# Performance work log

Measured on AMD Instinct MI355X. Metric: run time of the kernel, lower is better.

The kernel has to match this reference:

```python
import jax, jax.numpy as jnp
import numpy as np

KERNEL_EPSILON = 0.001


def setup_inputs() -> dict:
    key = jax.random.key(0)
    k1, k2, k3 = jax.random.split(key, 3)
    B, H, S, D = 4, 16, 4096, 64
    return {
        "query": jax.random.normal(k1, (B, H, S, D), dtype=jnp.float32),
        "key": jax.random.normal(k2, (B, H, S, D), dtype=jnp.float32),
        "value": jax.random.normal(k3, (B, H, S, D), dtype=jnp.float32),
        "mask": jnp.ones((B, S), dtype=jnp.float32),
    }


def reference(query, key, value, mask):
    # ReLU feature map + epsilon
    q = jax.nn.relu(query) + KERNEL_EPSILON          # [B,H,S,D]
    k = jax.nn.relu(key) + KERNEL_EPSILON            # [B,H,S,D]
    k = k * mask[:, None, :, None]                   # mask keys
    # kv: [B,H,D,E] = sum_s k[...,s,d] * v[...,s,e]  (done first: linear attention)
    kv = jnp.einsum("bhsd,bhse->bhde", k, value)
    numerator = jnp.einsum("bhsd,bhde->bhse", q, kv)  # [B,H,S,D]
    k_sum = jnp.sum(k, axis=-2)                       # [B,H,D]
    denominator = jnp.einsum("bhsd,bhd->bhs", q, k_sum)[..., None]
    return numerator / denominator
```

## Files before the change

kernel.cpp:

```cpp
#include <hip/hip_runtime.h>


namespace {
constexpr int kB = 4, kH = 16, kS = 4096, kD = 64;
constexpr int kBH = kB * kH;
constexpr float kEps = 0.001f;

constexpr int KVSZ = kD * kD;
constexpr int SEG  = KVSZ + kD;
constexpr int F4PS = SEG / 4;
}

__device__ __forceinline__ void async_cp16(const float* g, float* l) {
  __builtin_amdgcn_global_load_lds(
      (const __attribute__((address_space(1))) void*)g,
      (__attribute__((address_space(3))) void*)l, 16, 0, 0);
}

__global__ __launch_bounds__(256, 2)
void pa_kv_partial(const float* __restrict__ key, const float* __restrict__ value,
                   const float* __restrict__ mask, float* __restrict__ P, int ch1) {
  __shared__ float smemV[3 * 2048];
  __shared__ float smemK[4 * 512];
  __shared__ float msk[512];
  __shared__ float ksm[256];

  const int tid  = threadIdx.x;
  const int wid  = tid >> 6;
  const int lane = tid & 63;

  const int bh    = blockIdx.x / ch1;
  const int chunk = blockIdx.x - bh * ch1;
  const int b     = bh >> 4;
  const int rows  = kS / ch1;
  const int s0    = chunk * rows;
  const int tiles = rows >> 5;

  const float* kg = key   + (size_t)bh * kS * kD;
  const float* vg = value + (size_t)bh * kS * kD;
  const float* mb = mask  + (size_t)b * kS;

  for (int i = tid; i < rows; i += 256) msk[i] = mb[s0 + i];
  __syncthreads();

  float* ksT = smemK + wid * 512;
  float* v0b = smemV + wid * 512;
  float* v1b = smemV + 2048 + wid * 512;
  float* v2b = smemV + 4096 + wid * 512;

  const int lrow = lane >> 4;
  const int lcol = (lane & 15) << 2;
  const int ti   = lane >> 3;
  const int tj   = lane & 7;

  float acc[8][8];
#pragma unroll
  for (int i = 0; i < 8; ++i)
#pragma unroll
    for (int j = 0; j < 8; ++j) acc[i][j] = 0.f;
  float4 ksacc = make_float4(0.f, 0.f, 0.f, 0.f);

  const int r0 = wid * 8;
  float4 kqA0, kqA1, kqB0, kqB1;
  float mA0, mA1, mB0, mB1;

  async_cp16(vg + (size_t)(s0 + r0 + lrow) * kD + lcol, v0b);
  async_cp16(vg + (size_t)(s0 + r0 + 4 + lrow) * kD + lcol, v0b + 256);
  kqA0 = *(const float4*)(kg + (size_t)(s0 + r0 + lrow) * kD + lcol);
  kqA1 = *(const float4*)(kg + (size_t)(s0 + r0 + 4 + lrow) * kD + lcol);
  asm volatile("" ::: "memory");
  async_cp16(vg + (size_t)(s0 + r0 + 32 + lrow) * kD + lcol, v1b);
  async_cp16(vg + (size_t)(s0 + r0 + 36 + lrow) * kD + lcol, v1b + 256);
  kqB0 = *(const float4*)(kg + (size_t)(s0 + r0 + 32 + lrow) * kD + lcol);
  kqB1 = *(const float4*)(kg + (size_t)(s0 + r0 + 36 + lrow) * kD + lcol);
  asm volatile("" ::: "memory");
  mA0 = msk[r0 + lrow];      mA1 = msk[r0 + 4 + lrow];
  mB0 = msk[r0 + 32 + lrow]; mB1 = msk[r0 + 36 + lrow];

  int ts2 = s0 + r0 + 64;
  int to2 = r0 + 64;

#define PA_RND(KQ0, KQ1, M0, M1, WAITN, ISSUE)                                \
  {                                                                           \
    float4 kt0, kt1;                                                          \
    kt0.x = (fmaxf(KQ0.x, 0.f) + kEps) * M0;                                  \
    kt0.y = (fmaxf(KQ0.y, 0.f) + kEps) * M0;                                  \
    kt0.z = (fmaxf(KQ0.z, 0.f) + kEps) * M0;                                  \
    kt0.w = (fmaxf(KQ0.w, 0.f) + kEps) * M0;                                  \
    kt1.x = (fmaxf(KQ1.x, 0.f) + kEps) * M1;                                  \
    kt1.y = (fmaxf(KQ1.y, 0.f) + kEps) * M1;                                  \
    kt1.z = (fmaxf(KQ1.z, 0.f) + kEps) * M1;                                  \
    kt1.w = (fmaxf(KQ1.w, 0.f) + kEps) * M1;                                  \
    ksacc.x += kt0.x + kt1.x; ksacc.y += kt0.y + kt1.y;                       \
    ksacc.z += kt0.z + kt1.z; ksacc.w += kt0.w + kt1.w;                       \
    *(float4*)&ksT[lrow * 64 + lcol]       = kt0;                             \
    *(float4*)&ksT[(lrow + 4) * 64 + lcol] = kt1;                             \
    if (ISSUE) {                                                              \
      async_cp16(vg + (size_t)(ts2 + lrow) * kD + lcol, v2b);                 \
      async_cp16(vg + (size_t)(ts2 + 4 + lrow) * kD + lcol, v2b + 256);       \
      KQ0 = *(const float4*)(kg + (size_t)(ts2 + lrow) * kD + lcol);          \
      KQ1 = *(const float4*)(kg + (size_t)(ts2 + 4 + lrow) * kD + lcol);      \
      M0 = msk[to2 + lrow];  M1 = msk[to2 + 4 + lrow];                        \
      ts2 += 32; to2 += 32;                                                   \
    }                                                                         \
    asm volatile("s_waitcnt vmcnt(" #WAITN ")" ::: "memory");                 \
    _Pragma("unroll")                                                         \
    for (int ss = 0; ss < 8; ++ss) {                                          \
      const float4 kf0 = *(const float4*)&ksT[ss * 64 + 8 * ti];              \
      const float4 kf1 = *(const float4*)&ksT[ss * 64 + 8 * ti + 4];          \
      const float4 vf0 = *(const float4*)&v0b[ss * 64 + 8 * tj];              \
      const float4 vf1 = *(const float4*)&v0b[ss * 64 + 8 * tj + 4];          \
      const float ka[8] = {kf0.x, kf0.y, kf0.z, kf0.w,                        \
                           kf1.x, kf1.y, kf1.z, kf1.w};                       \
      const float va_[8] = {vf0.x, vf0.y, vf0.z, vf0.w,                       \
                            vf1.x, vf1.y, vf1.z, vf1.w};                      \
      _Pragma("unroll")                                                       \
      for (int i = 0; i < 8; ++i)                                             \
        _Pragma("unroll")                                                     \
        for (int j = 0; j < 8; ++j)                                           \
          acc[i][j] = fmaf(ka[i], va_[j], acc[i][j]);                         \
    }                                                                         \
    { float* rot_ = v0b; v0b = v1b; v1b = v2b; v2b = rot_; }                  \
  }

  for (int t = 0; t < tiles - 2; t += 2) {
    PA_RND(kqA0, kqA1, mA0, mA1, 8, true)
    PA_RND(kqB0, kqB1, mB0, mB1, 8, true)
  }
  PA_RND(kqA0, kqA1, mA0, mA1, 4, false)
  PA_RND(kqB0, kqB1, mB0, mB1, 0, false)
#undef PA_RND

  ksacc.x += __shfl_xor(ksacc.x, 16); ksacc.x += __shfl_xor(ksacc.x, 32);
  ksacc.y += __shfl_xor(ksacc.y, 16); ksacc.y += __shfl_xor(ksacc.y, 32);
  ksacc.z += __shfl_xor(ksacc.z, 16); ksacc.z += __shfl_xor(ksacc.z, 32);
  ksacc.w += __shfl_xor(ksacc.w, 16); ksacc.w += __shfl_xor(ksacc.w, 32);
  if (lane < 16) *(float4*)&ksm[wid * 64 + 4 * lane] = ksacc;

#pragma unroll
  for (int w = 0; w < 4; ++w) {
    __syncthreads();
    if (wid == w) {
#pragma unroll
      for (int i = 0; i < 8; ++i)
#pragma unroll
        for (int jj = 0; jj < 2; ++jj) {
          const int j = i * 2 + jj;
          float4 o = make_float4(acc[i][jj * 4 + 0], acc[i][jj * 4 + 1],
                                 acc[i][jj * 4 + 2], acc[i][jj * 4 + 3]);
          float* p = &smemV[(size_t)(j * 64 + lane) * 4];
          if (w != 0) {
            const float4 prev = *(const float4*)p;
            o.x += prev.x; o.y += prev.y; o.z += prev.z; o.w += prev.w;
          }
          *(float4*)p = o;
        }
    }
  }
  __syncthreads();

  float* Pd = P + (size_t)blockIdx.x * SEG;
#pragma unroll
  for (int i = 0; i < 4; ++i) {
    const int idx = tid + 256 * i;
    *(float4*)&Pd[(size_t)idx * 4] = *(const float4*)&smemV[(size_t)idx * 4];
  }
  if (tid < kD)
    Pd[KVSZ + tid] = ksm[tid] + ksm[64 + tid] + ksm[128 + tid] + ksm[192 + tid];
}

__global__ __launch_bounds__(256)
void pa_reduce(const float* __restrict__ P, float* __restrict__ R, int nseg) {
  const int gid = blockIdx.x * 256 + threadIdx.x;
  if (gid >= kBH * F4PS) return;
  const int bh  = gid / F4PS;
  const int pos = gid - bh * F4PS;

  const float* base = P + (size_t)bh * nseg * SEG + (size_t)pos * 4;
  float ax = 0.f, ay = 0.f, az = 0.f, aw = 0.f;
  for (int c = 0; c < nseg; ++c) {
    const float4 t = *(const float4*)(base + (size_t)c * SEG);
    ax += t.x; ay += t.y; az += t.z; aw += t.w;
  }

  int dpos;
  if (pos < KVSZ / 4) {
    const int j  = pos >> 6, ln = pos & 63;
    const int d  = 8 * (ln >> 3) + (j >> 1);
    const int e4 = 2 * (ln & 7) + (j & 1);
    dpos = d * 16 + e4;
  } else {
    dpos = pos;
  }
  *(float4*)&R[(size_t)bh * SEG + (size_t)dpos * 4] = make_float4(ax, ay, az, aw);
}

__global__ __launch_bounds__(256)
void pa_out(const float* __restrict__ query, const float* __restrict__ R,
            float* __restrict__ out) {
  __shared__ float ost[64 * 68];

  const int tid    = threadIdx.x;
  const int bh     = blockIdx.x >> 4;
  const int rowblk = blockIdx.x & 15;
  const int s      = rowblk * 256 + tid;

  const float* qrow = query + ((size_t)bh * kS + s) * kD;
  const float* Rb   = R + (size_t)bh * SEG;

  float4 acc[16];
#pragma unroll
  for (int e = 0; e < 16; ++e) acc[e] = make_float4(0.f, 0.f, 0.f, 0.f);
  float den = 0.f;

#pragma unroll 4
  for (int d4 = 0; d4 < 16; ++d4) {
    const float4 qv = *(const float4*)(qrow + 4 * d4);
    const float qd[4] = {fmaxf(qv.x, 0.f) + kEps, fmaxf(qv.y, 0.f) + kEps,
                         fmaxf(qv.z, 0.f) + kEps, fmaxf(qv.w, 0.f) + kEps};
#pragma unroll
    for (int dd = 0; dd < 4; ++dd) {
      const int d = 4 * d4 + dd;
      den = fmaf(qd[dd], Rb[KVSZ + d], den);
      const float* kvr = Rb + d * 64;
#pragma unroll
      for (int e = 0; e < 16; ++e) {
        acc[e].x = fmaf(qd[dd], kvr[4 * e + 0], acc[e].x);
        acc[e].y = fmaf(qd[dd], kvr[4 * e + 1], acc[e].y);
        acc[e].z = fmaf(qd[dd], kvr[4 * e + 2], acc[e].z);
        acc[e].w = fmaf(qd[dd], kvr[4 * e + 3], acc[e].w);
      }
    }
  }

  const float inv = 1.0f / den;
#pragma unroll
  for (int e = 0; e < 16; ++e) {
    acc[e].x *= inv; acc[e].y *= inv; acc[e].z *= inv; acc[e].w *= inv;
  }

  float* ob = out + ((size_t)bh * kS + (size_t)rowblk * 256) * kD;
  const int wid = tid >> 6, l = tid & 63;
  for (int bb = 0; bb < 4; ++bb) {
    if (wid == bb) {
#pragma unroll
      for (int e = 0; e < 16; ++e) *(float4*)&ost[l * 68 + 4 * e] = acc[e];
    }
    __syncthreads();
#pragma unroll
    for (int jj = 0; jj < 4; ++jj) {
      const int g = tid + 256 * jj;
      const int r = g >> 4, c = g & 15;
      *(float4*)&ob[(size_t)(bb * 64 + r) * kD + 4 * c] =
          *(const float4*)&ost[r * 68 + 4 * c];
    }
    __syncthreads();
  }
}

extern "C" void kernel_launch(void* const* d_in, const int* in_sizes, int n_in,
                              void* d_out, int out_size, void* d_ws, size_t ws_size,
                              hipStream_t stream) {
  const float* query = (const float*)d_in[0];
  const float* key   = (const float*)d_in[1];
  const float* value = (const float*)d_in[2];
  const float* mask  = (const float*)d_in[3];
  float* outp = (float*)d_out;

  auto need = [](int ch1) -> size_t {
    return (size_t)(kBH * ch1 + kBH) * SEG * sizeof(float);
  };
  int CH1 = 8;
  if (ws_size >= need(16)) CH1 = 16;

  float* P = (float*)d_ws;
  float* R = P + (size_t)kBH * CH1 * SEG;

  hipLaunchKernelGGL(pa_kv_partial, dim3(kBH * CH1), dim3(256), 0, stream,
                     key, value, mask, P, CH1);
  hipLaunchKernelGGL(pa_reduce, dim3((kBH * F4PS + 255) / 256), dim3(256), 0, stream,
                     P, R, CH1);
  hipLaunchKernelGGL(pa_out, dim3(kBH * 16), dim3(256), 0, stream,
                     query, R, outp);
}
```

Before: 282.0 us.

## Stream raw K and V via async LDS copies in a 4-deep per-wave ring

Replaces the register-staged key load plus LDS store with direct global-to-LDS async copies of both K and V into a 4-slot per-wave ring buffer of 16-row tiles. The ReLU, epsilon and mask transform moves into the inner FMA loop, where it is applied on the fly to values read from LDS. The key-sum becomes a per-lane scalar accumulation, so the shuffle reduction goes away. This removes VGPR staging and LDS write traffic and deepens prefetch, at the cost of redundant feature-map ALU work per outer-product step and an extra lgkmcnt wait before each issue.

```diff
diff --git a/kernel.cpp b/kernel.cpp
--- a/kernel.cpp
+++ b/kernel.cpp
@@ -20,8 +20,7 @@
 __global__ __launch_bounds__(256, 2)
 void pa_kv_partial(const float* __restrict__ key, const float* __restrict__ value,
                    const float* __restrict__ mask, float* __restrict__ P, int ch1) {
-  __shared__ float smemV[3 * 2048];
-  __shared__ float smemK[4 * 512];
+  __shared__ float smemU[8192];
   __shared__ float msk[512];
   __shared__ float ksm[256];
 
@@ -34,7 +33,7 @@
   const int b     = bh >> 4;
   const int rows  = kS / ch1;
   const int s0    = chunk * rows;
-  const int tiles = rows >> 5;
+  const int rounds = rows >> 4;
 
   const float* kg = key   + (size_t)bh * kS * kD;
   const float* vg = value + (size_t)bh * kS * kD;
@@ -43,75 +42,64 @@
   for (int i = tid; i < rows; i += 256) msk[i] = mb[s0 + i];
   __syncthreads();
 
-  float* ksT = smemK + wid * 512;
-  float* v0b = smemV + wid * 512;
-  float* v1b = smemV + 2048 + wid * 512;
-  float* v2b = smemV + 4096 + wid * 512;
-
-  const int lrow = lane >> 4;
-  const int lcol = (lane & 15) << 2;
-  const int ti   = lane >> 3;
-  const int tj   = lane & 7;
+  float* const ring = smemU + wid * 2048;
+#define RK(Pp) (ring + (Pp) * 512)
+#define RV(Pp) (ring + (Pp) * 512 + 256)
+
+  const int ti = lane >> 3;
+  const int tj = lane & 7;
+  const int rw = wid * 4;
 
   float acc[8][8];
 #pragma unroll
   for (int i = 0; i < 8; ++i)
 #pragma unroll
     for (int j = 0; j < 8; ++j) acc[i][j] = 0.f;
-  float4 ksacc = make_float4(0.f, 0.f, 0.f, 0.f);
-
-  const int r0 = wid * 8;
-  float4 kqA0, kqA1, kqB0, kqB1;
-  float mA0, mA1, mB0, mB1;
-
-  async_cp16(vg + (size_t)(s0 + r0 + lrow) * kD + lcol, v0b);
-  async_cp16(vg + (size_t)(s0 + r0 + 4 + lrow) * kD + lcol, v0b + 256);
-  kqA0 = *(const float4*)(kg + (size_t)(s0 + r0 + lrow) * kD + lcol);
-  kqA1 = *(const float4*)(kg + (size_t)(s0 + r0 + 4 + lrow) * kD + lcol);
-  asm volatile("" ::: "memory");
-  async_cp16(vg + (size_t)(s0 + r0 + 32 + lrow) * kD + lcol, v1b);
-  async_cp16(vg + (size_t)(s0 + r0 + 36 + lrow) * kD + lcol, v1b + 256);
-  kqB0 = *(const float4*)(kg + (size_t)(s0 + r0 + 32 + lrow) * kD + lcol);
-  kqB1 = *(const float4*)(kg + (size_t)(s0 + r0 + 36 + lrow) * kD + lcol);
-  asm volatile("" ::: "memory");
-  mA0 = msk[r0 + lrow];      mA1 = msk[r0 + 4 + lrow];
-  mB0 = msk[r0 + 32 + lrow]; mB1 = msk[r0 + 36 + lrow];
-
-  int ts2 = s0 + r0 + 64;
-  int to2 = r0 + 64;
-
-#define PA_RND(KQ0, KQ1, M0, M1, WAITN, ISSUE)                                \
+  float ksacc = 0.f;
+
+  {
+    const size_t g0 = (size_t)(s0 + rw) * kD + lane * 4;
+    async_cp16(kg + g0, RK(0));
+    async_cp16(vg + g0, RV(0));
+    asm volatile("" ::: "memory");
+    async_cp16(kg + g0 + 16 * kD, RK(1));
+    async_cp16(vg + g0 + 16 * kD, RV(1));
+    asm volatile("" ::: "memory");
+    async_cp16(kg + g0 + 32 * kD, RK(2));
+    async_cp16(vg + g0 + 32 * kD, RV(2));
+    asm volatile("" ::: "memory");
+  }
+
+#define PA_RND(Pp, RR, DO_ISSUE, WAITN)                                       \
   {                                                                           \
-    float4 kt0, kt1;                                                          \
-    kt0.x = (fmaxf(KQ0.x, 0.f) + kEps) * M0;                                  \
-    kt0.y = (fmaxf(KQ0.y, 0.f) + kEps) * M0;                                  \
-    kt0.z = (fmaxf(KQ0.z, 0.f) + kEps) * M0;                                  \
-    kt0.w = (fmaxf(KQ0.w, 0.f) + kEps) * M0;                                  \
-    kt1.x = (fmaxf(KQ1.x, 0.f) + kEps) * M1;                                  \
-    kt1.y = (fmaxf(KQ1.y, 0.f) + kEps) * M1;                                  \
-    kt1.z = (fmaxf(KQ1.z, 0.f) + kEps) * M1;                                  \
-    kt1.w = (fmaxf(KQ1.w, 0.f) + kEps) * M1;                                  \
-    ksacc.x += kt0.x + kt1.x; ksacc.y += kt0.y + kt1.y;                       \
-    ksacc.z += kt0.z + kt1.z; ksacc.w += kt0.w + kt1.w;                       \
-    *(float4*)&ksT[lrow * 64 + lcol]       = kt0;                             \
-    *(float4*)&ksT[(lrow + 4) * 64 + lcol] = kt1;                             \
-    if (ISSUE) {                                                              \
-      async_cp16(vg + (size_t)(ts2 + lrow) * kD + lcol, v2b);                 \
-      async_cp16(vg + (size_t)(ts2 + 4 + lrow) * kD + lcol, v2b + 256);       \
-      KQ0 = *(const float4*)(kg + (size_t)(ts2 + lrow) * kD + lcol);          \
-      KQ1 = *(const float4*)(kg + (size_t)(ts2 + 4 + lrow) * kD + lcol);      \
-      M0 = msk[to2 + lrow];  M1 = msk[to2 + 4 + lrow];                        \
-      ts2 += 32; to2 += 32;                                                   \
+    if (DO_ISSUE) {                                                           \
+      asm volatile("s_waitcnt lgkmcnt(0)" ::: "memory");                      \
+      const size_t gi = (size_t)(s0 + ((RR) + 3) * 16 + rw) * kD + lane * 4;  \
+      async_cp16(kg + gi, RK(((Pp) + 3) & 3));                                \
+      async_cp16(vg + gi, RV(((Pp) + 3) & 3));                                \
     }                                                                         \
     asm volatile("s_waitcnt vmcnt(" #WAITN ")" ::: "memory");                 \
+    const float* Ks = RK(Pp);                                                 \
+    const float* Vs = RV(Pp);                                                 \
+    const int rb = (RR) * 16 + rw;                                            \
     _Pragma("unroll")                                                         \
-    for (int ss = 0; ss < 8; ++ss) {                                          \
-      const float4 kf0 = *(const float4*)&ksT[ss * 64 + 8 * ti];              \
-      const float4 kf1 = *(const float4*)&ksT[ss * 64 + 8 * ti + 4];          \
-      const float4 vf0 = *(const float4*)&v0b[ss * 64 + 8 * tj];              \
-      const float4 vf1 = *(const float4*)&v0b[ss * 64 + 8 * tj + 4];          \
-      const float ka[8] = {kf0.x, kf0.y, kf0.z, kf0.w,                        \
-                           kf1.x, kf1.y, kf1.z, kf1.w};                       \
+    for (int ss = 0; ss < 4; ++ss) {                                          \
+      const float m  = msk[rb + ss];                                          \
+      const float em = kEps * m;                                              \
+      ksacc += fmaf(fmaxf(Ks[ss * 64 + lane], 0.f), m, em);                   \
+      const float4 kf0 = *(const float4*)&Ks[ss * 64 + 8 * ti];               \
+      const float4 kf1 = *(const float4*)&Ks[ss * 64 + 8 * ti + 4];           \
+      const float4 vf0 = *(const float4*)&Vs[ss * 64 + 8 * tj];               \
+      const float4 vf1 = *(const float4*)&Vs[ss * 64 + 8 * tj + 4];           \
+      float ka[8];                                                            \
+      ka[0] = fmaf(fmaxf(kf0.x, 0.f), m, em);                                 \
+      ka[1] = fmaf(fmaxf(kf0.y, 0.f), m, em);                                 \
+      ka[2] = fmaf(fmaxf(kf0.z, 0.f), m, em);                                 \
+      ka[3] = fmaf(fmaxf(kf0.w, 0.f), m, em);                                 \
+      ka[4] = fmaf(fmaxf(kf1.x, 0.f), m, em);                                 \
+      ka[5] = fmaf(fmaxf(kf1.y, 0.f), m, em);                                 \
+      ka[6] = fmaf(fmaxf(kf1.z, 0.f), m, em);                                 \
+      ka[7] = fmaf(fmaxf(kf1.w, 0.f), m, em);                                 \
       const float va_[8] = {vf0.x, vf0.y, vf0.z, vf0.w,                       \
                             vf1.x, vf1.y, vf1.z, vf1.w};                      \
       _Pragma("unroll")                                                       \
@@ -120,22 +108,24 @@
         for (int j = 0; j < 8; ++j)                                           \
           acc[i][j] = fmaf(ka[i], va_[j], acc[i][j]);                         \
     }                                                                         \
-    { float* rot_ = v0b; v0b = v1b; v1b = v2b; v2b = rot_; }                  \
-  }
-
-  for (int t = 0; t < tiles - 2; t += 2) {
-    PA_RND(kqA0, kqA1, mA0, mA1, 8, true)
-    PA_RND(kqB0, kqB1, mB0, mB1, 8, true)
-  }
-  PA_RND(kqA0, kqA1, mA0, mA1, 4, false)
-  PA_RND(kqB0, kqB1, mB0, mB1, 0, false)
+  }
+
+  int t = 0;
+  for (; t < rounds - 7; t += 4) {
+    PA_RND(0, t + 0, true, 6)
+    PA_RND(1, t + 1, true, 6)
+    PA_RND(2, t + 2, true, 6)
+    PA_RND(3, t + 3, true, 6)
+  }
+  PA_RND(0, t + 0, true, 6)
+  PA_RND(1, t + 1, false, 4)
+  PA_RND(2, t + 2, false, 2)
+  PA_RND(3, t + 3, false, 0)
 #undef PA_RND
-
-  ksacc.x += __shfl_xor(ksacc.x, 16); ksacc.x += __shfl_xor(ksacc.x, 32);
-  ksacc.y += __shfl_xor(ksacc.y, 16); ksacc.y += __shfl_xor(ksacc.y, 32);
-  ksacc.z += __shfl_xor(ksacc.z, 16); ksacc.z += __shfl_xor(ksacc.z, 32);
-  ksacc.w += __shfl_xor(ksacc.w, 16); ksacc.w += __shfl_xor(ksacc.w, 32);
-  if (lane < 16) *(float4*)&ksm[wid * 64 + 4 * lane] = ksacc;
+#undef RK
+#undef RV
+
+  ksm[wid * 64 + lane] = ksacc;
 
 #pragma unroll
   for (int w = 0; w < 4; ++w) {
@@ -148,7 +138,7 @@
           const int j = i * 2 + jj;
           float4 o = make_float4(acc[i][jj * 4 + 0], acc[i][jj * 4 + 1],
                                  acc[i][jj * 4 + 2], acc[i][jj * 4 + 3]);
-          float* p = &smemV[(size_t)(j * 64 + lane) * 4];
+          float* p = &smemU[(size_t)(j * 64 + lane) * 4];
           if (w != 0) {
             const float4 prev = *(const float4*)p;
             o.x += prev.x; o.y += prev.y; o.z += prev.z; o.w += prev.w;
@@ -163,7 +153,7 @@
 #pragma unroll
   for (int i = 0; i < 4; ++i) {
     const int idx = tid + 256 * i;
-    *(float4*)&Pd[(size_t)idx * 4] = *(const float4*)&smemV[(size_t)idx * 4];
+    *(float4*)&Pd[(size_t)idx * 4] = *(const float4*)&smemU[(size_t)idx * 4];
   }
   if (tid < kD)
     Pd[KVSZ + tid] = ksm[tid] + ksm[64 + tid] + ksm[128 + tid] + ksm[192 + tid];
```

Measured after the change: 288.9 us. 2.5% more time.

## Replace async LDS triple-buffering of V with register prefetch of K and V

Applied to the files above, without the earlier changes.

Drops the global_load_lds async copies and three-slot rotating V buffers in favour of loading both K and V into registers two tiles ahead and storing them into a single per-wave LDS tile each round. Explicit vmcnt waits are removed so the compiler schedules the waits. Launch bounds change from 2 blocks per CU minimum to 1, which lets the compiler use more registers for the extra prefetched V values but may lower occupancy. Per-wave smem is smaller, and there is no barrier between the LDS writes and the reads of other lanes because each wave owns its own tile.

```diff
diff --git a/kernel.cpp b/kernel.cpp
--- a/kernel.cpp
+++ b/kernel.cpp
@@ -11,17 +11,10 @@
 constexpr int F4PS = SEG / 4;
 }
 
-__device__ __forceinline__ void async_cp16(const float* g, float* l) {
-  __builtin_amdgcn_global_load_lds(
-      (const __attribute__((address_space(1))) void*)g,
-      (__attribute__((address_space(3))) void*)l, 16, 0, 0);
-}
-
-__global__ __launch_bounds__(256, 2)
+__global__ __launch_bounds__(256, 1)
 void pa_kv_partial(const float* __restrict__ key, const float* __restrict__ value,
                    const float* __restrict__ mask, float* __restrict__ P, int ch1) {
-  __shared__ float smemV[3 * 2048];
-  __shared__ float smemK[4 * 512];
+  __shared__ float smem[4096];
   __shared__ float msk[512];
   __shared__ float ksm[256];
 
@@ -36,17 +29,15 @@
   const int s0    = chunk * rows;
   const int tiles = rows >> 5;
 
-  const float* kg = key   + (size_t)bh * kS * kD;
-  const float* vg = value + (size_t)bh * kS * kD;
+  const float* kb = key   + (size_t)bh * kS * kD;
+  const float* vb = value + (size_t)bh * kS * kD;
   const float* mb = mask  + (size_t)b * kS;
 
   for (int i = tid; i < rows; i += 256) msk[i] = mb[s0 + i];
   __syncthreads();
 
-  float* ksT = smemK + wid * 512;
-  float* v0b = smemV + wid * 512;
-  float* v1b = smemV + 2048 + wid * 512;
-  float* v2b = smemV + 4096 + wid * 512;
+  float* ksT = smem + wid * 1024;
+  float* vsT = smem + wid * 1024 + 512;
 
   const int lrow = lane >> 4;
   const int lcol = (lane & 15) << 2;
@@ -60,56 +51,57 @@
     for (int j = 0; j < 8; ++j) acc[i][j] = 0.f;
   float4 ksacc = make_float4(0.f, 0.f, 0.f, 0.f);
 
-  const int r0 = wid * 8;
-  float4 kqA0, kqA1, kqB0, kqB1;
-  float mA0, mA1, mB0, mB1;
-
-  async_cp16(vg + (size_t)(s0 + r0 + lrow) * kD + lcol, v0b);
-  async_cp16(vg + (size_t)(s0 + r0 + 4 + lrow) * kD + lcol, v0b + 256);
-  kqA0 = *(const float4*)(kg + (size_t)(s0 + r0 + lrow) * kD + lcol);
-  kqA1 = *(const float4*)(kg + (size_t)(s0 + r0 + 4 + lrow) * kD + lcol);
-  asm volatile("" ::: "memory");
-  async_cp16(vg + (size_t)(s0 + r0 + 32 + lrow) * kD + lcol, v1b);
-  async_cp16(vg + (size_t)(s0 + r0 + 36 + lrow) * kD + lcol, v1b + 256);
-  kqB0 = *(const float4*)(kg + (size_t)(s0 + r0 + 32 + lrow) * kD + lcol);
-  kqB1 = *(const float4*)(kg + (size_t)(s0 + r0 + 36 + lrow) * kD + lcol);
-  asm volatile("" ::: "memory");
-  mA0 = msk[r0 + lrow];      mA1 = msk[r0 + 4 + lrow];
-  mB0 = msk[r0 + 32 + lrow]; mB1 = msk[r0 + 36 + lrow];
-
-  int ts2 = s0 + r0 + 64;
-  int to2 = r0 + 64;
-
-#define PA_RND(KQ0, KQ1, M0, M1, WAITN, ISSUE)                                \
+  const size_t eoff0 = (size_t)(lrow)     * kD + lcol;
+  const size_t eoff1 = (size_t)(lrow + 4) * kD + lcol;
+  const int    trow  = wid * 8;
+
+  const float* kt0p = kb + (size_t)(s0 + trow) * kD;
+  const float* vt0p = vb + (size_t)(s0 + trow) * kD;
+  float4 kqA0 = *(const float4*)(kt0p + eoff0);
+  float4 kqA1 = *(const float4*)(kt0p + eoff1);
+  float4 vqA0 = *(const float4*)(vt0p + eoff0);
+  float4 vqA1 = *(const float4*)(vt0p + eoff1);
+  float4 kqB0 = *(const float4*)(kt0p + 32 * kD + eoff0);
+  float4 kqB1 = *(const float4*)(kt0p + 32 * kD + eoff1);
+  float4 vqB0 = *(const float4*)(vt0p + 32 * kD + eoff0);
+  float4 vqB1 = *(const float4*)(vt0p + 32 * kD + eoff1);
+
+#define PA_RND(KQ0, KQ1, VQ0, VQ1, TT)                                        \
   {                                                                           \
+    const int rb = (TT) * 32 + trow;                                          \
+    const float m0 = msk[rb + lrow];                                          \
+    const float m1 = msk[rb + 4 + lrow];                                      \
     float4 kt0, kt1;                                                          \
-    kt0.x = (fmaxf(KQ0.x, 0.f) + kEps) * M0;                                  \
-    kt0.y = (fmaxf(KQ0.y, 0.f) + kEps) * M0;                                  \
-    kt0.z = (fmaxf(KQ0.z, 0.f) + kEps) * M0;                                  \
-    kt0.w = (fmaxf(KQ0.w, 0.f) + kEps) * M0;                                  \
-    kt1.x = (fmaxf(KQ1.x, 0.f) + kEps) * M1;                                  \
-    kt1.y = (fmaxf(KQ1.y, 0.f) + kEps) * M1;                                  \
-    kt1.z = (fmaxf(KQ1.z, 0.f) + kEps) * M1;                                  \
-    kt1.w = (fmaxf(KQ1.w, 0.f) + kEps) * M1;                                  \
-    ksacc.x += kt0.x + kt1.x; ksacc.y += kt0.y + kt1.y;                       \
-    ksacc.z += kt0.z + kt1.z; ksacc.w += kt0.w + kt1.w;                       \
+    kt0.x = (fmaxf(KQ0.x, 0.f) + kEps) * m0;                                  \
+    kt0.y = (fmaxf(KQ0.y, 0.f) + kEps) * m0;                                  \
+    kt0.z = (fmaxf(KQ0.z, 0.f) + kEps) * m0;                                  \
+    kt0.w = (fmaxf(KQ0.w, 0.f) + kEps) * m0;                                  \
+    kt1.x = (fmaxf(KQ1.x, 0.f) + kEps) * m1;                                  \
+    kt1.y = (fmaxf(KQ1.y, 0.f) + kEps) * m1;                                  \
+    kt1.z = (fmaxf(KQ1.z, 0.f) + kEps) * m1;                                  \
+    kt1.w = (fmaxf(KQ1.w, 0.f) + kEps) * m1;                                  \
+    ksacc.x += kt0.x + kt1.x;                                                 \
+    ksacc.y += kt0.y + kt1.y;                                                 \
+    ksacc.z += kt0.z + kt1.z;                                                 \
+    ksacc.w += kt0.w + kt1.w;                                                 \
     *(float4*)&ksT[lrow * 64 + lcol]       = kt0;                             \
     *(float4*)&ksT[(lrow + 4) * 64 + lcol] = kt1;                             \
-    if (ISSUE) {                                                              \
-      async_cp16(vg + (size_t)(ts2 + lrow) * kD + lcol, v2b);                 \
-      async_cp16(vg + (size_t)(ts2 + 4 + lrow) * kD + lcol, v2b + 256);       \
-      KQ0 = *(const float4*)(kg + (size_t)(ts2 + lrow) * kD + lcol);          \
-      KQ1 = *(const float4*)(kg + (size_t)(ts2 + 4 + lrow) * kD + lcol);      \
-      M0 = msk[to2 + lrow];  M1 = msk[to2 + 4 + lrow];                        \
-      ts2 += 32; to2 += 32;                                                   \
+    *(float4*)&vsT[lrow * 64 + lcol]       = VQ0;                             \
+    *(float4*)&vsT[(lrow + 4) * 64 + lcol] = VQ1;                             \
+    if ((TT) + 2 < tiles) {                                                   \
+      const float* kn = kb + (size_t)(s0 + ((TT) + 2) * 32 + trow) * kD;      \
+      const float* vn = vb + (size_t)(s0 + ((TT) + 2) * 32 + trow) * kD;      \
+      KQ0 = *(const float4*)(kn + eoff0);                                     \
+      KQ1 = *(const float4*)(kn + eoff1);                                     \
+      VQ0 = *(const float4*)(vn + eoff0);                                     \
+      VQ1 = *(const float4*)(vn + eoff1);                                     \
     }                                                                         \
-    asm volatile("s_waitcnt vmcnt(" #WAITN ")" ::: "memory");                 \
     _Pragma("unroll")                                                         \
     for (int ss = 0; ss < 8; ++ss) {                                          \
       const float4 kf0 = *(const float4*)&ksT[ss * 64 + 8 * ti];              \
       const float4 kf1 = *(const float4*)&ksT[ss * 64 + 8 * ti + 4];          \
-      const float4 vf0 = *(const float4*)&v0b[ss * 64 + 8 * tj];              \
-      const float4 vf1 = *(const float4*)&v0b[ss * 64 + 8 * tj + 4];          \
+      const float4 vf0 = *(const float4*)&vsT[ss * 64 + 8 * tj];              \
+      const float4 vf1 = *(const float4*)&vsT[ss * 64 + 8 * tj + 4];          \
       const float ka[8] = {kf0.x, kf0.y, kf0.z, kf0.w,                        \
                            kf1.x, kf1.y, kf1.z, kf1.w};                       \
       const float va_[8] = {vf0.x, vf0.y, vf0.z, vf0.w,                       \
@@ -120,15 +112,12 @@
         for (int j = 0; j < 8; ++j)                                           \
           acc[i][j] = fmaf(ka[i], va_[j], acc[i][j]);                         \
     }                                                                         \
-    { float* rot_ = v0b; v0b = v1b; v1b = v2b; v2b = rot_; }                  \
-  }
-
-  for (int t = 0; t < tiles - 2; t += 2) {
-    PA_RND(kqA0, kqA1, mA0, mA1, 8, true)
-    PA_RND(kqB0, kqB1, mB0, mB1, 8, true)
-  }
-  PA_RND(kqA0, kqA1, mA0, mA1, 4, false)
-  PA_RND(kqB0, kqB1, mB0, mB1, 0, false)
+  }
+
+  for (int t = 0; t < tiles; t += 2) {
+    PA_RND(kqA0, kqA1, vqA0, vqA1, t)
+    PA_RND(kqB0, kqB1, vqB0, vqB1, t + 1)
+  }
 #undef PA_RND
 
   ksacc.x += __shfl_xor(ksacc.x, 16); ksacc.x += __shfl_xor(ksacc.x, 32);
@@ -148,7 +137,7 @@
           const int j = i * 2 + jj;
           float4 o = make_float4(acc[i][jj * 4 + 0], acc[i][jj * 4 + 1],
                                  acc[i][jj * 4 + 2], acc[i][jj * 4 + 3]);
-          float* p = &smemV[(size_t)(j * 64 + lane) * 4];
+          float* p = &smem[(size_t)(j * 64 + lane) * 4];
           if (w != 0) {
             const float4 prev = *(const float4*)p;
             o.x += prev.x; o.y += prev.y; o.z += prev.z; o.w += prev.w;
@@ -163,7 +152,7 @@
 #pragma unroll
   for (int i = 0; i < 4; ++i) {
     const int idx = tid + 256 * i;
-    *(float4*)&Pd[(size_t)idx * 4] = *(const float4*)&smemV[(size_t)idx * 4];
+    *(float4*)&Pd[(size_t)idx * 4] = *(const float4*)&smem[(size_t)idx * 4];
   }
   if (tid < kD)
     Pd[KVSZ + tid] = ksm[tid] + ksm[64 + tid] + ksm[128 + tid] + ksm[192 + tid];
```

Measured after the change: 257.5 us. 1.1x faster.
